# Kernel tuning notes

Hardware: AMD Instinct MI355X
Metric: run time of the kernel (lower is better)

Reference implementation:

```python
import jax, jax.numpy as jnp
import numpy as np

SCALES = (1, 3, 6)
PRECISION = 10  # pywt default: 2**10 samples of psi on [-5, 5]


def _gaus1_filters():
    """Replicates pywt.cwt's integrated-wavelet filters for wavelet='gaus1'.

    pywt: psi, x = wavelet.wavefun(10); int_psi = cumsum(psi)*step; per scale a:
    j = arange(a*(x[-1]-x[0])+1)/(a*step) -> int indices; filter = int_psi[j][::-1];
    conv = np.convolve(data, filter). np.convolve flips its kernel, so the
    equivalent cross-correlation kernel (lax.conv semantics) is int_psi[j].
    """
    x = np.linspace(-5.0, 5.0, 2 ** PRECISION)
    step = x[1] - x[0]
    psi = -2.0 * x * np.exp(-x ** 2) / (np.pi / 2.0) ** 0.25
    int_psi = np.cumsum(psi) * step
    filts = []
    for a in SCALES:
        j = (np.arange(a * (x[-1] - x[0]) + 1) / (a * step)).astype(np.int64)
        j = j[j < int_psi.size]
        filts.append(int_psi[j].astype(np.float32))  # correlation kernel
    return filts

_FILTS = _gaus1_filters()


def setup_inputs() -> dict:
    key = jax.random.key(0)
    x = jax.random.normal(key, (32, 4096, 64), dtype=jnp.float32)
    return {"x": x}


def reference(x):
    B, S, C = x.shape
    sig = jnp.transpose(x, (0, 2, 1)).reshape(B * C, 1, S)  # [B*C, 1, S]
    outs = []
    for a, f in zip(SCALES, _FILTS):
        L = f.shape[0]
        k = jnp.asarray(f).reshape(1, 1, L)
        # full convolution (np.convolve): pad L-1 both sides
        conv = jax.lax.conv_general_dilated(
            sig, k, window_strides=(1,), padding=[(L - 1, L - 1)],
            dimension_numbers=("NCH", "OIH", "NCH"))  # [B*C, 1, S+L-1]
        coef = -np.sqrt(a).astype(np.float32) * jnp.diff(conv, axis=-1)  # [B*C,1,S+L-2]
        d = (coef.shape[-1] - S) / 2.0
        coef = coef[..., int(np.floor(d)): coef.shape[-1] - int(np.ceil(d))]  # [B*C,1,S]
        outs.append(coef)
    out = jnp.concatenate(outs, axis=1).reshape(B, C, len(SCALES), S)
    return jnp.transpose(out, (0, 2, 3, 1))  # [B, 3, S, C]
```

## Files before the change

### kernel.cpp

```cpp
#include <hip/hip_runtime.h>
#include <math.h>

#define S_LEN  4096
#define NCH    64
#define TILE_S 128
#define RPT    16
#define TY     8
#define HALO_L 31
#define STAGE  (TILE_S + 61)

__device__ float g_wt[112];

__global__ void cwt_setup() {
  __shared__ double ip[1024];
  __shared__ double tsum[64];
  const int t = threadIdx.x;
  const double delta = 10.0 / 1023.0;
  const double step  = (-5.0 + delta) + 5.0;
  const double cnorm = pow(3.141592653589793 * 0.5, 0.25);

  double local[16];
  double s = 0.0;
  #pragma unroll
  for (int i = 0; i < 16; ++i) {
    const int idx = t * 16 + i;
    const double p  = (double)idx * delta;
    const double xi = (idx == 1023) ? 5.0 : (p - 5.0);
    const double psi = (-2.0 * xi) * exp(-(xi * xi)) / cnorm;
    s += psi;
    local[i] = s;
  }
  tsum[t] = s;
  __syncthreads();
  double off = 0.0;
  for (int k = 0; k < t; ++k) off += tsum[k];
  #pragma unroll
  for (int i = 0; i < 16; ++i) ip[t * 16 + i] = (local[i] + off) * step;
  __syncthreads();

  const int as_[3]  = {6, 3, 1};
  const int lf_[3]  = {61, 31, 11};
  const int ofs_[3] = {0, 62, 94};
  for (int si = 0; si < 3; ++si) {
    const double denom = (double)as_[si] * step;
    const float  sqa   = (float)sqrt((double)as_[si]);
    const int    lf    = lf_[si];
    for (int tt = t; tt <= lf; tt += 64) {
      float km1 = 0.f, kt = 0.f;
      if (tt >= 1)      km1 = (float)ip[(long)(((double)(tt - 1)) / denom)];
      if (tt <= lf - 1) kt  = (float)ip[(long)(((double)tt) / denom)];
      g_wt[ofs_[si] + tt] = -sqa * (km1 - kt);
    }
  }
}

__global__ __launch_bounds__(512)
void cwt_main(const float* __restrict__ x, float* __restrict__ out) {
  __shared__ float lds[STAGE * NCH];
  const int c   = threadIdx.x;
  const int ty  = threadIdx.y;
  const int tid = ty * 64 + c;
  const int b   = blockIdx.y;
  const int s0  = blockIdx.x * TILE_S;
  const float* xb = x + (size_t)b * S_LEN * NCH;
  const int row0 = s0 - HALO_L;

  for (int idx = tid; idx < STAGE * 16; idx += TY * 64) {
    const int r = idx >> 4, q = idx & 15;
    const int row = row0 + r;
    float4 v = make_float4(0.f, 0.f, 0.f, 0.f);
    if (row >= 0 && row < S_LEN)
      v = *(const float4*)(xb + ((size_t)row * NCH + (q << 2)));
    *(float4*)(&lds[r * NCH + (q << 2)]) = v;
  }
  __syncthreads();

  const int base = ty * RPT;
  float win[61 + RPT];
  #pragma unroll
  for (int u = 0; u < 61 + RPT; ++u) win[u] = lds[(base + u) * NCH + c];

  float* outb = out + (size_t)b * 3 * S_LEN * NCH;
  const int srow = s0 + base;

  {
    float acc[RPT];
    #pragma unroll
    for (int r = 0; r < RPT; ++r) acc[r] = 0.f;
    #pragma unroll
    for (int t = 0; t < 62; ++t) {
      const float wv = g_wt[t];
      #pragma unroll
      for (int r = 0; r < RPT; ++r) acc[r] += wv * win[t + r];
    }
    float* o = outb + ((size_t)(2 * S_LEN + srow)) * NCH + c;
    #pragma unroll
    for (int r = 0; r < RPT; ++r) o[(size_t)r * NCH] = acc[r];
  }
  {
    float acc[RPT];
    #pragma unroll
    for (int r = 0; r < RPT; ++r) acc[r] = 0.f;
    #pragma unroll
    for (int t = 0; t < 32; ++t) {
      const float wv = g_wt[62 + t];
      #pragma unroll
      for (int r = 0; r < RPT; ++r) acc[r] += wv * win[t + 15 + r];
    }
    float* o = outb + ((size_t)(1 * S_LEN + srow)) * NCH + c;
    #pragma unroll
    for (int r = 0; r < RPT; ++r) o[(size_t)r * NCH] = acc[r];
  }
  {
    float acc[RPT];
    #pragma unroll
    for (int r = 0; r < RPT; ++r) acc[r] = 0.f;
    #pragma unroll
    for (int t = 0; t < 12; ++t) {
      const float wv = g_wt[94 + t];
      #pragma unroll
      for (int r = 0; r < RPT; ++r) acc[r] += wv * win[t + 25 + r];
    }
    float* o = outb + ((size_t)srow) * NCH + c;
    #pragma unroll
    for (int r = 0; r < RPT; ++r) o[(size_t)r * NCH] = acc[r];
  }
}

extern "C" void kernel_launch(void* const* d_in, const int* in_sizes, int n_in,
                              void* d_out, int out_size, void* d_ws, size_t ws_size,
                              hipStream_t stream) {
  (void)n_in; (void)out_size; (void)d_ws; (void)ws_size;
  const float* x = (const float*)d_in[0];
  float* out = (float*)d_out;
  const int B = in_sizes[0] / (S_LEN * NCH);

  hipLaunchKernelGGL(cwt_setup, dim3(1), dim3(64), 0, stream);
  dim3 grid(S_LEN / TILE_S, B);
  dim3 block(NCH, TY);
  hipLaunchKernelGGL(cwt_main, grid, block, 0, stream, x, out);
}
```

Baseline: 143.8 us.

## Fuse filter-weight setup into main CWT kernel and vectorise weight loads

Removes the separate single-block setup kernel. Every block now computes the integrated gaus1 wavelet with a wave-level shuffle scan and builds the filter weights in shared memory, while its input tile loads are in flight in registers. Weights are read as float4 from LDS rather than as scalar global loads. This saves one launch and the serialized setup, at the cost of redundant double-precision exp work in every block and extra LDS and register pressure. The scale-3 and scale-1 weight offsets are realigned to 64 and 96 to allow the vector loads.

```diff
diff --git a/kernel.cpp b/kernel.cpp
--- a/kernel.cpp
+++ b/kernel.cpp
@@ -9,54 +9,13 @@
 #define HALO_L 31
 #define STAGE  (TILE_S + 61)
 
-__device__ float g_wt[112];
+__global__ __launch_bounds__(512)
+void cwt_fused(const float* __restrict__ x, float* __restrict__ out) {
+  __shared__ __align__(16) float lds[STAGE * NCH];
+  __shared__ __align__(16) float wt[112];
+  __shared__ float ipf[1024];
+  __shared__ double wsum[TY];
 
-__global__ void cwt_setup() {
-  __shared__ double ip[1024];
-  __shared__ double tsum[64];
-  const int t = threadIdx.x;
-  const double delta = 10.0 / 1023.0;
-  const double step  = (-5.0 + delta) + 5.0;
-  const double cnorm = pow(3.141592653589793 * 0.5, 0.25);
-
-  double local[16];
-  double s = 0.0;
-  #pragma unroll
-  for (int i = 0; i < 16; ++i) {
-    const int idx = t * 16 + i;
-    const double p  = (double)idx * delta;
-    const double xi = (idx == 1023) ? 5.0 : (p - 5.0);
-    const double psi = (-2.0 * xi) * exp(-(xi * xi)) / cnorm;
-    s += psi;
-    local[i] = s;
-  }
-  tsum[t] = s;
-  __syncthreads();
-  double off = 0.0;
-  for (int k = 0; k < t; ++k) off += tsum[k];
-  #pragma unroll
-  for (int i = 0; i < 16; ++i) ip[t * 16 + i] = (local[i] + off) * step;
-  __syncthreads();
-
-  const int as_[3]  = {6, 3, 1};
-  const int lf_[3]  = {61, 31, 11};
-  const int ofs_[3] = {0, 62, 94};
-  for (int si = 0; si < 3; ++si) {
-    const double denom = (double)as_[si] * step;
-    const float  sqa   = (float)sqrt((double)as_[si]);
-    const int    lf    = lf_[si];
-    for (int tt = t; tt <= lf; tt += 64) {
-      float km1 = 0.f, kt = 0.f;
-      if (tt >= 1)      km1 = (float)ip[(long)(((double)(tt - 1)) / denom)];
-      if (tt <= lf - 1) kt  = (float)ip[(long)(((double)tt) / denom)];
-      g_wt[ofs_[si] + tt] = -sqa * (km1 - kt);
-    }
-  }
-}
-
-__global__ __launch_bounds__(512)
-void cwt_main(const float* __restrict__ x, float* __restrict__ out) {
-  __shared__ float lds[STAGE * NCH];
   const int c   = threadIdx.x;
   const int ty  = threadIdx.y;
   const int tid = ty * 64 + c;
@@ -65,13 +24,66 @@
   const float* xb = x + (size_t)b * S_LEN * NCH;
   const int row0 = s0 - HALO_L;
 
-  for (int idx = tid; idx < STAGE * 16; idx += TY * 64) {
+  float4 stg[6];
+  #pragma unroll
+  for (int i = 0; i < 6; ++i) {
+    const int idx = tid + i * 512;
     const int r = idx >> 4, q = idx & 15;
     const int row = row0 + r;
     float4 v = make_float4(0.f, 0.f, 0.f, 0.f);
-    if (row >= 0 && row < S_LEN)
+    if (idx < STAGE * 16 && row >= 0 && row < S_LEN)
       v = *(const float4*)(xb + ((size_t)row * NCH + (q << 2)));
-    *(float4*)(&lds[r * NCH + (q << 2)]) = v;
+    stg[i] = v;
+  }
+
+  const double delta = 10.0 / 1023.0;
+  const double step  = (-5.0 + delta) + 5.0;
+  const double cnorm = pow(3.141592653589793 * 0.5, 0.25);
+
+  const int i0 = 2 * tid, i1 = 2 * tid + 1;
+  const double x0 = (i0 == 1023) ? 5.0 : ((double)i0 * delta - 5.0);
+  const double x1 = (i1 == 1023) ? 5.0 : ((double)i1 * delta - 5.0);
+  const double p0 = (-2.0 * x0) * exp(-(x0 * x0)) / cnorm;
+  const double p1 = (-2.0 * x1) * exp(-(x1 * x1)) / cnorm;
+  const double s2 = p0 + p1;
+
+  double inc = s2;
+  #pragma unroll
+  for (int off = 1; off < 64; off <<= 1) {
+    const double u = __shfl_up(inc, (unsigned)off, 64);
+    if (c >= off) inc += u;
+  }
+  if (c == 63) wsum[ty] = inc;
+  __syncthreads();
+
+  double pre = 0.0;
+  #pragma unroll
+  for (int k = 0; k < TY; ++k) if (k < ty) pre += wsum[k];
+  const double excl = pre + (inc - s2);
+  ipf[i0] = (float)((excl + p0) * step);
+  ipf[i1] = (float)((excl + p0 + p1) * step);
+  __syncthreads();
+
+  {
+    int a = 0, ofs = 0, lf = 0, t = 0, live = 0;
+    if (tid < 62)                   { a = 6; ofs = 0;  lf = 61; t = tid;      live = 1; }
+    else if (tid >= 64 && tid < 96) { a = 3; ofs = 64; lf = 31; t = tid - 64; live = 1; }
+    else if (tid >= 96 && tid < 108){ a = 1; ofs = 96; lf = 11; t = tid - 96; live = 1; }
+    if (live) {
+      const double denom = (double)a * step;
+      const float  sqa   = (float)sqrt((double)a);
+      float km1 = 0.f, kt = 0.f;
+      if (t >= 1)      km1 = ipf[(int)(long)(((double)(t - 1)) / denom)];
+      if (t <= lf - 1) kt  = ipf[(int)(long)(((double)t) / denom)];
+      wt[ofs + t] = -sqa * (km1 - kt);
+    }
+  }
+
+  #pragma unroll
+  for (int i = 0; i < 6; ++i) {
+    const int idx = tid + i * 512;
+    if (idx < STAGE * 16)
+      *(float4*)(&lds[(idx >> 4) * NCH + ((idx & 15) << 2)]) = stg[i];
   }
   __syncthreads();
 
@@ -82,16 +94,25 @@
 
   float* outb = out + (size_t)b * 3 * S_LEN * NCH;
   const int srow = s0 + base;
+  const float4* wt4 = (const float4*)wt;
 
   {
     float acc[RPT];
     #pragma unroll
     for (int r = 0; r < RPT; ++r) acc[r] = 0.f;
     #pragma unroll
-    for (int t = 0; t < 62; ++t) {
-      const float wv = g_wt[t];
+    for (int t4 = 0; t4 < 15; ++t4) {
+      const float4 w4 = wt4[t4];
       #pragma unroll
-      for (int r = 0; r < RPT; ++r) acc[r] += wv * win[t + r];
+      for (int r = 0; r < RPT; ++r)
+        acc[r] += w4.x * win[4 * t4 + r]     + w4.y * win[4 * t4 + 1 + r]
+                + w4.z * win[4 * t4 + 2 + r] + w4.w * win[4 * t4 + 3 + r];
+    }
+    {
+      const float2 w2 = *(const float2*)&wt[60];
+      #pragma unroll
+      for (int r = 0; r < RPT; ++r)
+        acc[r] += w2.x * win[60 + r] + w2.y * win[61 + r];
     }
     float* o = outb + ((size_t)(2 * S_LEN + srow)) * NCH + c;
     #pragma unroll
@@ -102,10 +123,12 @@
     #pragma unroll
     for (int r = 0; r < RPT; ++r) acc[r] = 0.f;
     #pragma unroll
-    for (int t = 0; t < 32; ++t) {
-      const float wv = g_wt[62 + t];
+    for (int t4 = 0; t4 < 8; ++t4) {
+      const float4 w4 = wt4[16 + t4];
       #pragma unroll
-      for (int r = 0; r < RPT; ++r) acc[r] += wv * win[t + 15 + r];
+      for (int r = 0; r < RPT; ++r)
+        acc[r] += w4.x * win[4 * t4 + 15 + r] + w4.y * win[4 * t4 + 16 + r]
+                + w4.z * win[4 * t4 + 17 + r] + w4.w * win[4 * t4 + 18 + r];
     }
     float* o = outb + ((size_t)(1 * S_LEN + srow)) * NCH + c;
     #pragma unroll
@@ -116,10 +139,12 @@
     #pragma unroll
     for (int r = 0; r < RPT; ++r) acc[r] = 0.f;
     #pragma unroll
-    for (int t = 0; t < 12; ++t) {
-      const float wv = g_wt[94 + t];
+    for (int t4 = 0; t4 < 3; ++t4) {
+      const float4 w4 = wt4[24 + t4];
       #pragma unroll
-      for (int r = 0; r < RPT; ++r) acc[r] += wv * win[t + 25 + r];
+      for (int r = 0; r < RPT; ++r)
+        acc[r] += w4.x * win[4 * t4 + 25 + r] + w4.y * win[4 * t4 + 26 + r]
+                + w4.z * win[4 * t4 + 27 + r] + w4.w * win[4 * t4 + 28 + r];
     }
     float* o = outb + ((size_t)srow) * NCH + c;
     #pragma unroll
@@ -135,8 +160,7 @@
   float* out = (float*)d_out;
   const int B = in_sizes[0] / (S_LEN * NCH);
 
-  hipLaunchKernelGGL(cwt_setup, dim3(1), dim3(64), 0, stream);
   dim3 grid(S_LEN / TILE_S, B);
   dim3 block(NCH, TY);
-  hipLaunchKernelGGL(cwt_main, grid, block, 0, stream, x, out);
+  hipLaunchKernelGGL(cwt_fused, grid, block, 0, stream, x, out);
 }
```

New measurement: 135.3 us. 6.0% less time.

## Pass filter weights as kernel args, fuse three scales with rolling register window

Applied to the files above, without the earlier changes.

The setup kernel launch is removed. The filter weights are now computed on the host and passed by value as kernel arguments, so they live in constant/scalar registers instead of global memory. The three per-scale convolutions are merged into one pass over the taps that reuses a 20-entry rolling register window loaded from LDS. This replaces the earlier 77-entry window and aims to cut register pressure so occupancy can rise (launch_bounds 512,4). Global loads are also batched into registers before the LDS stores, and outputs are written per scale in order.

```diff
diff --git a/kernel.cpp b/kernel.cpp
--- a/kernel.cpp
+++ b/kernel.cpp
@@ -9,54 +9,13 @@
 #define HALO_L 31
 #define STAGE  (TILE_S + 61)
 
-__device__ float g_wt[112];
+struct WtArgs { float w6[62]; float w3[32]; float w1[12]; };
 
-__global__ void cwt_setup() {
-  __shared__ double ip[1024];
-  __shared__ double tsum[64];
-  const int t = threadIdx.x;
-  const double delta = 10.0 / 1023.0;
-  const double step  = (-5.0 + delta) + 5.0;
-  const double cnorm = pow(3.141592653589793 * 0.5, 0.25);
+__global__ __launch_bounds__(512, 4)
+void cwt_main(const float* __restrict__ x, float* __restrict__ out,
+              const WtArgs W) {
+  __shared__ __align__(16) float lds[STAGE * NCH];
 
-  double local[16];
-  double s = 0.0;
-  #pragma unroll
-  for (int i = 0; i < 16; ++i) {
-    const int idx = t * 16 + i;
-    const double p  = (double)idx * delta;
-    const double xi = (idx == 1023) ? 5.0 : (p - 5.0);
-    const double psi = (-2.0 * xi) * exp(-(xi * xi)) / cnorm;
-    s += psi;
-    local[i] = s;
-  }
-  tsum[t] = s;
-  __syncthreads();
-  double off = 0.0;
-  for (int k = 0; k < t; ++k) off += tsum[k];
-  #pragma unroll
-  for (int i = 0; i < 16; ++i) ip[t * 16 + i] = (local[i] + off) * step;
-  __syncthreads();
-
-  const int as_[3]  = {6, 3, 1};
-  const int lf_[3]  = {61, 31, 11};
-  const int ofs_[3] = {0, 62, 94};
-  for (int si = 0; si < 3; ++si) {
-    const double denom = (double)as_[si] * step;
-    const float  sqa   = (float)sqrt((double)as_[si]);
-    const int    lf    = lf_[si];
-    for (int tt = t; tt <= lf; tt += 64) {
-      float km1 = 0.f, kt = 0.f;
-      if (tt >= 1)      km1 = (float)ip[(long)(((double)(tt - 1)) / denom)];
-      if (tt <= lf - 1) kt  = (float)ip[(long)(((double)tt) / denom)];
-      g_wt[ofs_[si] + tt] = -sqa * (km1 - kt);
-    }
-  }
-}
-
-__global__ __launch_bounds__(512)
-void cwt_main(const float* __restrict__ x, float* __restrict__ out) {
-  __shared__ float lds[STAGE * NCH];
   const int c   = threadIdx.x;
   const int ty  = threadIdx.y;
   const int tid = ty * 64 + c;
@@ -65,66 +24,64 @@
   const float* xb = x + (size_t)b * S_LEN * NCH;
   const int row0 = s0 - HALO_L;
 
-  for (int idx = tid; idx < STAGE * 16; idx += TY * 64) {
+  float4 stg[6];
+  #pragma unroll
+  for (int i = 0; i < 6; ++i) {
+    const int idx = tid + i * 512;
     const int r = idx >> 4, q = idx & 15;
     const int row = row0 + r;
     float4 v = make_float4(0.f, 0.f, 0.f, 0.f);
-    if (row >= 0 && row < S_LEN)
+    if (idx < STAGE * 16 && row >= 0 && row < S_LEN)
       v = *(const float4*)(xb + ((size_t)row * NCH + (q << 2)));
-    *(float4*)(&lds[r * NCH + (q << 2)]) = v;
+    stg[i] = v;
+  }
+  #pragma unroll
+  for (int i = 0; i < 6; ++i) {
+    const int idx = tid + i * 512;
+    if (idx < STAGE * 16)
+      *(float4*)(&lds[(idx >> 4) * NCH + ((idx & 15) << 2)]) = stg[i];
   }
   __syncthreads();
 
   const int base = ty * RPT;
-  float win[61 + RPT];
+  const float* col = &lds[base * NCH + c];
+
+  float win[20];
   #pragma unroll
-  for (int u = 0; u < 61 + RPT; ++u) win[u] = lds[(base + u) * NCH + c];
+  for (int k = 0; k < 19; ++k) win[k] = col[k * NCH];
 
-  float* outb = out + (size_t)b * 3 * S_LEN * NCH;
+  float a6[RPT], a3[RPT], a1[RPT];
+  #pragma unroll
+  for (int r = 0; r < RPT; ++r) { a6[r] = 0.f; a3[r] = 0.f; a1[r] = 0.f; }
+
+  #pragma unroll
+  for (int t = 0; t < 62; ++t) {
+    if (t < 58) win[(t + 19) % 20] = col[(t + 19) * NCH];
+    const float c6 = W.w6[t];
+    #pragma unroll
+    for (int r = 0; r < RPT; ++r) a6[r] += c6 * win[(t + r) % 20];
+    if (t >= 15 && t <= 46) {
+      const float c3 = W.w3[t - 15];
+      #pragma unroll
+      for (int r = 0; r < RPT; ++r) a3[r] += c3 * win[(t + r) % 20];
+    }
+    if (t >= 25 && t <= 36) {
+      const float c1 = W.w1[t - 25];
+      #pragma unroll
+      for (int r = 0; r < RPT; ++r) a1[r] += c1 * win[(t + r) % 20];
+    }
+  }
+
   const int srow = s0 + base;
-
-  {
-    float acc[RPT];
-    #pragma unroll
-    for (int r = 0; r < RPT; ++r) acc[r] = 0.f;
-    #pragma unroll
-    for (int t = 0; t < 62; ++t) {
-      const float wv = g_wt[t];
-      #pragma unroll
-      for (int r = 0; r < RPT; ++r) acc[r] += wv * win[t + r];
-    }
-    float* o = outb + ((size_t)(2 * S_LEN + srow)) * NCH + c;
-    #pragma unroll
-    for (int r = 0; r < RPT; ++r) o[(size_t)r * NCH] = acc[r];
-  }
-  {
-    float acc[RPT];
-    #pragma unroll
-    for (int r = 0; r < RPT; ++r) acc[r] = 0.f;
-    #pragma unroll
-    for (int t = 0; t < 32; ++t) {
-      const float wv = g_wt[62 + t];
-      #pragma unroll
-      for (int r = 0; r < RPT; ++r) acc[r] += wv * win[t + 15 + r];
-    }
-    float* o = outb + ((size_t)(1 * S_LEN + srow)) * NCH + c;
-    #pragma unroll
-    for (int r = 0; r < RPT; ++r) o[(size_t)r * NCH] = acc[r];
-  }
-  {
-    float acc[RPT];
-    #pragma unroll
-    for (int r = 0; r < RPT; ++r) acc[r] = 0.f;
-    #pragma unroll
-    for (int t = 0; t < 12; ++t) {
-      const float wv = g_wt[94 + t];
-      #pragma unroll
-      for (int r = 0; r < RPT; ++r) acc[r] += wv * win[t + 25 + r];
-    }
-    float* o = outb + ((size_t)srow) * NCH + c;
-    #pragma unroll
-    for (int r = 0; r < RPT; ++r) o[(size_t)r * NCH] = acc[r];
-  }
+  float* o = out + (((size_t)b * 3) * S_LEN + srow) * NCH + c;
+  #pragma unroll
+  for (int r = 0; r < RPT; ++r) o[(size_t)r * NCH] = a1[r];
+  o += (size_t)S_LEN * NCH;
+  #pragma unroll
+  for (int r = 0; r < RPT; ++r) o[(size_t)r * NCH] = a3[r];
+  o += (size_t)S_LEN * NCH;
+  #pragma unroll
+  for (int r = 0; r < RPT; ++r) o[(size_t)r * NCH] = a6[r];
 }
 
 extern "C" void kernel_launch(void* const* d_in, const int* in_sizes, int n_in,
@@ -135,8 +92,36 @@
   float* out = (float*)d_out;
   const int B = in_sizes[0] / (S_LEN * NCH);
 
-  hipLaunchKernelGGL(cwt_setup, dim3(1), dim3(64), 0, stream);
+  WtArgs W;
+  {
+    static double ip[1024];
+    const double delta = 10.0 / 1023.0;
+    const double step  = (-5.0 + delta) + 5.0;
+    const double cn    = pow(3.141592653589793 * 0.5, 0.25);
+    double s = 0.0;
+    for (int i = 0; i < 1024; ++i) {
+      const double xi  = (i == 1023) ? 5.0 : ((double)i * delta - 5.0);
+      const double psi = (-2.0 * xi) * exp(-(xi * xi)) / cn;
+      s += psi;
+      ip[i] = s * step;
+    }
+    const int   as_[3] = {6, 3, 1};
+    const int   lf_[3] = {61, 31, 11};
+    float*      wp_[3] = {W.w6, W.w3, W.w1};
+    for (int si = 0; si < 3; ++si) {
+      const double denom = (double)as_[si] * step;
+      const float  sqa   = (float)sqrt((double)as_[si]);
+      const int    lf    = lf_[si];
+      for (int t = 0; t <= lf; ++t) {
+        float km1 = 0.f, kt = 0.f;
+        if (t >= 1)      km1 = (float)ip[(long)(((double)(t - 1)) / denom)];
+        if (t <= lf - 1) kt  = (float)ip[(long)(((double)t) / denom)];
+        wp_[si][t] = -sqa * (km1 - kt);
+      }
+    }
+  }
+
   dim3 grid(S_LEN / TILE_S, B);
   dim3 block(NCH, TY);
-  hipLaunchKernelGGL(cwt_main, grid, block, 0, stream, x, out);
+  hipLaunchKernelGGL(cwt_main, grid, block, 0, stream, x, out, W);
 }
```

After: 202.8 us. +41.0%, slower.
